# Optimization experiments

Measured on AMD Instinct MI355X. Metric: run time of the kernel, lower is better.

Reference implementation:

```python
import jax, jax.numpy as jnp
from jax import lax
import numpy as np

B, T, H, P = 256, 2048, 256, 24

def setup_inputs() -> dict:
    key = jax.random.key(0)
    ks = jax.random.split(key, 7)
    s_ih = 1.0 / np.sqrt(H)
    return {
        "x": jax.random.normal(ks[0], (B, T, 1), dtype=jnp.float32),
        "W_ih": jax.random.normal(ks[1], (H, 1), dtype=jnp.float32) * s_ih,
        "W_hh": jax.random.normal(ks[2], (H, H), dtype=jnp.float32) * s_ih,
        "b_ih": jax.random.normal(ks[3], (H,), dtype=jnp.float32) * s_ih,
        "b_hh": jax.random.normal(ks[4], (H,), dtype=jnp.float32) * s_ih,
        "W_out": jax.random.normal(ks[5], (P, H), dtype=jnp.float32) * s_ih,
        "b_out": jax.random.normal(ks[6], (P,), dtype=jnp.float32) * s_ih,
    }

def reference(x, W_ih, W_hh, b_ih, b_hh, W_out, b_out):
    # Precompute input projection for all timesteps: [B,T,H]
    xp = jnp.einsum('bti,hi->bth', x, W_ih) + b_ih + b_hh
    h0 = jnp.zeros((x.shape[0], W_hh.shape[0]), dtype=x.dtype)

    def step(h, xt):  # xt: [B,H]
        h_new = jnp.tanh(xt + h @ W_hh.T)
        return h_new, None

    hT, _ = lax.scan(step, h0, xp.transpose(1, 0, 2))  # scan over T
    # Linear head on last hidden state: [B,P]
    return hT @ W_out.T + b_out
```

## Files before the change

### kernel.cpp

```cpp
#include <hip/hip_runtime.h>


#define BB 256
#define TT 2048
#define HH 256
#define PP 24
#define HSTR 20

typedef float v2f __attribute__((ext_vector_type(2)));

__device__ __forceinline__ int hidx(int k) { return (k >> 4) * HSTR + (k & 15); }

template<int CTRL>
__device__ __forceinline__ float dppadd(float dst, float src) {
    return dst + __int_as_float(__builtin_amdgcn_update_dpp(
        0, __float_as_int(src), CTRL, 0xf, 0xf, true));
}

__global__ __launch_bounds__(512, 2)
void rnn_persist(const float* __restrict__ x,
                 const float* __restrict__ W_ih,
                 const float* __restrict__ W_hh,
                 const float* __restrict__ b_ih,
                 const float* __restrict__ b_hh,
                 const float* __restrict__ W_out,
                 const float* __restrict__ b_out,
                 float* __restrict__ out)
{
    __shared__ __align__(16) float hbuf[2][16 * HSTR];

    const int tid = threadIdx.x;
    const int b   = blockIdx.x;
    const int c   = tid & 15;
    const int g   = tid >> 4;

    if (tid < HH) hbuf[0][hidx(tid)] = 0.0f;

    const int m[8] = {0, 2, 7, 5, 8, 10, 15, 13};

    v2f w2[8][8];
    #pragma unroll
    for (int s = 0; s < 8; ++s) {
        const int row_idx = 8 * g + ((c ^ m[s]) >> 1);
        const float* row = W_hh + row_idx * HH + 16 * c;
        #pragma unroll
        for (int j = 0; j < 4; ++j) {
            const float4 q = *(const float4*)(row + 4 * j);
            w2[s][2 * j + 0] = (v2f){q.x, q.y};
            w2[s][2 * j + 1] = (v2f){q.z, q.w};
        }
    }

    const int   o_fin = 8 * g + (c >> 1);
    const float wih   = W_ih[o_fin];
    const float cb    = b_ih[o_fin] + b_hh[o_fin];
    const int   widx  = hidx(o_fin);
    const bool  writer = (c & 1) == 0;

    __syncthreads();

    const float* hc0 = hbuf[0] + c * HSTR;
    const float* hc1 = hbuf[1] + c * HSTR;
    const float* xb  = x + b * TT;

    auto step = [&](const float* __restrict__ cur, float* __restrict__ nxt,
                    float xt) __attribute__((always_inline)) {
        const float4* h4p = (const float4*)cur;
        const float4 qa = h4p[0], qb = h4p[1], qc = h4p[2], qd = h4p[3];
        v2f h2[8];
        h2[0] = (v2f){qa.x, qa.y}; h2[1] = (v2f){qa.z, qa.w};
        h2[2] = (v2f){qb.x, qb.y}; h2[3] = (v2f){qb.z, qb.w};
        h2[4] = (v2f){qc.x, qc.y}; h2[5] = (v2f){qc.z, qc.w};
        h2[6] = (v2f){qd.x, qd.y}; h2[7] = (v2f){qd.z, qd.w};

        float aa[8];
        #pragma unroll
        for (int s = 0; s < 8; ++s) {
            v2f acc = w2[s][0] * h2[0];
            #pragma unroll
            for (int j = 1; j < 8; ++j)
                acc = __builtin_elementwise_fma(w2[s][j], h2[j], acc);
            aa[s] = acc.x + acc.y;
        }

        float b0 = dppadd<0x128>(aa[0], aa[4]);
        float b1 = dppadd<0x128>(aa[1], aa[5]);
        float b2 = dppadd<0x128>(aa[2], aa[6]);
        float b3 = dppadd<0x128>(aa[3], aa[7]);
        float c0 = dppadd<0x141>(b0, b2);
        float c1 = dppadd<0x141>(b1, b3);
        float d  = dppadd<0x4E>(c0, c1);
        float e  = dppadd<0xB1>(d, d);

        const float u  = fmaf(xt, wih, cb) + e;
        const float p  = __builtin_amdgcn_exp2f(u * 2.8853900817779268f);
        const float th = fmaf(-2.f, __builtin_amdgcn_rcpf(p + 1.f), 1.f);
        if (writer) nxt[widx] = th;
        __syncthreads();
    };

    for (int t = 0; t < TT; t += 4) {
        const float x0 = xb[t + 0];
        const float x1 = xb[t + 1];
        const float x2 = xb[t + 2];
        const float x3 = xb[t + 3];
        step(hc0, hbuf[1], x0);
        step(hc1, hbuf[0], x1);
        step(hc0, hbuf[1], x2);
        step(hc1, hbuf[0], x3);
    }

    if (tid < PP) {
        const float* wo = W_out + tid * HH;
        float s0 = 0.f, s1 = 0.f, s2 = 0.f, s3 = 0.f;
        #pragma unroll
        for (int h = 0; h < HH; h += 4) {
            s0 = fmaf(wo[h + 0], hbuf[0][hidx(h + 0)], s0);
            s1 = fmaf(wo[h + 1], hbuf[0][hidx(h + 1)], s1);
            s2 = fmaf(wo[h + 2], hbuf[0][hidx(h + 2)], s2);
            s3 = fmaf(wo[h + 3], hbuf[0][hidx(h + 3)], s3);
        }
        out[b * PP + tid] = b_out[tid] + (s0 + s1) + (s2 + s3);
    }
}

extern "C" void kernel_launch(void* const* d_in, const int* in_sizes, int n_in,
                              void* d_out, int out_size, void* d_ws, size_t ws_size,
                              hipStream_t stream) {
    const float* x     = (const float*)d_in[0];
    const float* W_ih  = (const float*)d_in[1];
    const float* W_hh  = (const float*)d_in[2];
    const float* b_ih  = (const float*)d_in[3];
    const float* b_hh  = (const float*)d_in[4];
    const float* W_out = (const float*)d_in[5];
    const float* b_out = (const float*)d_in[6];
    float* out = (float*)d_out;

    rnn_persist<<<BB, 512, 0, stream>>>(x, W_ih, W_hh, b_ih, b_hh, W_out, b_out, out);
}
```

Measured before the change: 1.041 ms.

## Halve threads per block so each thread computes a full output row

After: 1.344 ms. 1.29x slower.

```diff
diff --git a/kernel.cpp b/kernel.cpp
--- a/kernel.cpp
+++ b/kernel.cpp
@@ -17,7 +17,7 @@
         0, __float_as_int(src), CTRL, 0xf, 0xf, true));
 }
 
-__global__ __launch_bounds__(512, 2)
+__global__ __launch_bounds__(256, 1)
 void rnn_persist(const float* __restrict__ x,
                  const float* __restrict__ W_ih,
                  const float* __restrict__ W_hh,
@@ -34,14 +34,14 @@
     const int c   = tid & 15;
     const int g   = tid >> 4;
 
-    if (tid < HH) hbuf[0][hidx(tid)] = 0.0f;
+    hbuf[0][hidx(tid)] = 0.0f;
 
-    const int m[8] = {0, 2, 7, 5, 8, 10, 15, 13};
+    const int m[16] = {0, 1, 2, 3, 7, 6, 5, 4, 8, 9, 10, 11, 15, 14, 13, 12};
 
-    v2f w2[8][8];
+    v2f w2[16][8];
     #pragma unroll
-    for (int s = 0; s < 8; ++s) {
-        const int row_idx = 8 * g + ((c ^ m[s]) >> 1);
+    for (int s = 0; s < 16; ++s) {
+        const int row_idx = 16 * g + (c ^ m[s]);
         const float* row = W_hh + row_idx * HH + 16 * c;
         #pragma unroll
         for (int j = 0; j < 4; ++j) {
@@ -51,11 +51,9 @@
         }
     }
 
-    const int   o_fin = 8 * g + (c >> 1);
-    const float wih   = W_ih[o_fin];
-    const float cb    = b_ih[o_fin] + b_hh[o_fin];
-    const int   widx  = hidx(o_fin);
-    const bool  writer = (c & 1) == 0;
+    const float wih  = W_ih[tid];
+    const float cb   = b_ih[tid] + b_hh[tid];
+    const int   widx = hidx(tid);
 
     __syncthreads();
 
@@ -73,9 +71,9 @@
         h2[4] = (v2f){qc.x, qc.y}; h2[5] = (v2f){qc.z, qc.w};
         h2[6] = (v2f){qd.x, qd.y}; h2[7] = (v2f){qd.z, qd.w};
 
-        float aa[8];
+        float aa[16];
         #pragma unroll
-        for (int s = 0; s < 8; ++s) {
+        for (int s = 0; s < 16; ++s) {
             v2f acc = w2[s][0] * h2[0];
             #pragma unroll
             for (int j = 1; j < 8; ++j)
@@ -83,19 +81,21 @@
             aa[s] = acc.x + acc.y;
         }
 
-        float b0 = dppadd<0x128>(aa[0], aa[4]);
-        float b1 = dppadd<0x128>(aa[1], aa[5]);
-        float b2 = dppadd<0x128>(aa[2], aa[6]);
-        float b3 = dppadd<0x128>(aa[3], aa[7]);
-        float c0 = dppadd<0x141>(b0, b2);
-        float c1 = dppadd<0x141>(b1, b3);
-        float d  = dppadd<0x4E>(c0, c1);
-        float e  = dppadd<0xB1>(d, d);
+        float bb[8];
+        #pragma unroll
+        for (int i = 0; i < 8; ++i) bb[i] = dppadd<0x128>(aa[i], aa[i + 8]);
+        float cc[4];
+        #pragma unroll
+        for (int i = 0; i < 4; ++i) cc[i] = dppadd<0x141>(bb[i], bb[i + 4]);
+        float dd[2];
+        #pragma unroll
+        for (int i = 0; i < 2; ++i) dd[i] = dppadd<0x4E>(cc[i], cc[i + 2]);
+        const float e = dppadd<0xB1>(dd[0], dd[1]);
 
         const float u  = fmaf(xt, wih, cb) + e;
         const float p  = __builtin_amdgcn_exp2f(u * 2.8853900817779268f);
         const float th = fmaf(-2.f, __builtin_amdgcn_rcpf(p + 1.f), 1.f);
-        if (writer) nxt[widx] = th;
+        nxt[widx] = th;
         __syncthreads();
     };
 
@@ -136,5 +136,5 @@
     const float* b_out = (const float*)d_in[6];
     float* out = (float*)d_out;
 
-    rnn_persist<<<BB, 512, 0, stream>>>(x, W_ih, W_hh, b_ih, b_hh, W_out, b_out, out);
+    rnn_persist<<<BB, 256, 0, stream>>>(x, W_ih, W_hh, b_ih, b_hh, W_out, b_out, out);
 }
```
